# Kernel optimization log

Measured on AMD Instinct MI355X. Metric: run time of the kernel, lower is better.

The kernel has to match this reference:

```python
import jax, jax.numpy as jnp
import numpy as np
from jax import lax

B, S, E, SD = 8, 4096, 1024, 8


def setup_inputs() -> dict:
    key = jax.random.key(0)
    ks = jax.random.split(key, 4)
    x = jax.random.normal(ks[0], (B, S, E), dtype=jnp.float32)
    W_in = jax.random.normal(ks[1], (E, E + SD), dtype=jnp.float32) / np.sqrt(E)
    b_in = jnp.zeros((E + SD,), dtype=jnp.float32)
    W_g = jax.random.normal(ks[2], (E + SD, SD), dtype=jnp.float32) / np.sqrt(E + SD)
    b_g = jnp.zeros((SD,), dtype=jnp.float32)
    W_out = jax.random.normal(ks[3], (E + SD, E), dtype=jnp.float32) / np.sqrt(E + SD)
    b_out = jnp.zeros((E,), dtype=jnp.float32)
    return {"x": x, "W_in": W_in, "b_in": b_in, "W_g": W_g, "b_g": b_g,
            "W_out": W_out, "b_out": b_out}


def reference(x, W_in, b_in, W_g, b_g, W_out, b_out):
    embed_dim = W_in.shape[0]
    # State-independent projections batched over the whole sequence.
    combined = jnp.einsum('bse,ec->bsc', x, W_in) + b_in            # [B,S,E+SD]
    embed = combined[..., :embed_dim]                                # [B,S,E]
    state_in = combined[..., embed_dim:]                             # [B,S,SD]
    gate = jax.nn.sigmoid(jnp.einsum('bsc,cd->bsd', combined, W_g) + b_g)  # [B,S,SD]

    # Only the tiny gated state recurrence is sequential.
    def step(state, gs):
        g, si = gs
        new = g * state + (1.0 - g) * si
        return new, new

    state0 = jnp.zeros((x.shape[0], state_in.shape[-1]), dtype=x.dtype)
    g_t = jnp.moveaxis(gate, 1, 0)        # [S,B,SD]
    si_t = jnp.moveaxis(state_in, 1, 0)   # [S,B,SD]
    final_state, states = lax.scan(step, state0, (g_t, si_t))
    states = jnp.moveaxis(states, 0, 1)   # [B,S,SD]

    out = jnp.einsum('bsc,cd->bsd', jnp.concatenate([embed, states], axis=-1), W_out) + b_out
    return out, final_state
```

## Files before the change

kernel.cpp:

```cpp
#include <hip/hip_runtime.h>

typedef unsigned short ushort_t;
typedef __attribute__((ext_vector_type(8))) short short8;
typedef __attribute__((ext_vector_type(4))) float floatx4;

#define B_ 8
#define S_ 4096
#define E_ 1024
#define SD_ 8
#define M_TOTAL (B_ * S_)
#define NC 1032
#define NPAD 1152

__device__ __forceinline__ ushort_t f2bf(float f) {
    union { float f; unsigned u; } v; v.f = f;
    unsigned u = v.u;
    unsigned r = (u + 0x7fffu + ((u >> 16) & 1u)) >> 16;
    return (ushort_t)r;
}
__device__ __forceinline__ float bf2f(ushort_t h) {
    union { unsigned u; float f; } v; v.u = ((unsigned)h) << 16;
    return v.f;
}

__device__ __forceinline__ void stage16(ushort_t* lds_base_uniform, const ushort_t* g) {
#if __has_builtin(__builtin_amdgcn_global_load_lds)
    __builtin_amdgcn_global_load_lds(
        (const __attribute__((address_space(1))) void*)g,
        (__attribute__((address_space(3))) void*)lds_base_uniform, 16, 0, 0);
#else
    int lane = threadIdx.x & 63;
    *(short8*)((ushort_t*)lds_base_uniform + lane * 8) = *(const short8*)g;
#endif
}

__global__ void cvt_x4(const float* __restrict__ x, ushort_t* __restrict__ xb) {
    size_t i = ((size_t)blockIdx.x * 256 + threadIdx.x) * 4;
    float4 v = *(const float4*)(x + i);
    ushort4 o;
    o.x = f2bf(v.x); o.y = f2bf(v.y); o.z = f2bf(v.z); o.w = f2bf(v.w);
    *(ushort4*)(xb + i) = o;
}

__global__ void prep_win(const float* __restrict__ W, ushort_t* __restrict__ WT) {
    int idx = blockIdx.x * 256 + threadIdx.x;
    int n = idx >> 10, k = idx & 1023;
    WT[idx] = (n < NC) ? f2bf(W[(size_t)k * NC + n]) : (ushort_t)0;
}

__global__ void prep_wout(const float* __restrict__ W, ushort_t* __restrict__ WT) {
    int idx = blockIdx.x * 256 + threadIdx.x;
    int n = idx / NPAD, k = idx - n * NPAD;
    WT[idx] = (k < NC) ? f2bf(W[(size_t)k * E_ + n]) : (ushort_t)0;
}

template <bool OUT_BF16>
__global__ __launch_bounds__(256, 2) void gemm_bt(
    const ushort_t* __restrict__ A, const ushort_t* __restrict__ BT,
    void* __restrict__ Cout, const float* __restrict__ bias,
    int K, int lda, int ldb, int ldc, int nbias)
{
    __shared__ __align__(16) ushort_t sA[128 * 32];
    __shared__ __align__(16) ushort_t sB[128 * 32];
    const int tid = threadIdx.x;
    const int wave = tid >> 6;
    const int lane = tid & 63;
    const int m0 = blockIdx.y * 128;
    const int n0 = blockIdx.x * 128;
    const int wm = wave >> 1, wn = wave & 1;
    const int fr = lane & 15, fq = lane >> 4;
    const int sr = lane >> 2;
    const int sc = (lane & 3) * 8;

    floatx4 acc[4][4];
#pragma unroll
    for (int i = 0; i < 4; i++)
#pragma unroll
        for (int j = 0; j < 4; j++) acc[i][j] = (floatx4)0.f;

    const ushort_t* gA = A + (size_t)(m0 + wave * 32 + sr) * lda + sc;
    const ushort_t* gB = BT + (size_t)(n0 + wave * 32 + sr) * ldb + sc;

    for (int k0 = 0; k0 < K; k0 += 32) {
        __syncthreads();
        stage16(&sA[(wave * 32 + 0) * 32], gA + k0);
        stage16(&sA[(wave * 32 + 16) * 32], gA + (size_t)16 * lda + k0);
        stage16(&sB[(wave * 32 + 0) * 32], gB + k0);
        stage16(&sB[(wave * 32 + 16) * 32], gB + (size_t)16 * ldb + k0);
        __syncthreads();

        short8 a[4], b[4];
#pragma unroll
        for (int i = 0; i < 4; i++)
            a[i] = *(const short8*)&sA[(wm * 64 + i * 16 + fr) * 32 + fq * 8];
#pragma unroll
        for (int j = 0; j < 4; j++)
            b[j] = *(const short8*)&sB[(wn * 64 + j * 16 + fr) * 32 + fq * 8];
#pragma unroll
        for (int i = 0; i < 4; i++)
#pragma unroll
            for (int j = 0; j < 4; j++)
                acc[i][j] = __builtin_amdgcn_mfma_f32_16x16x32_bf16(a[i], b[j], acc[i][j], 0, 0, 0);
    }

#pragma unroll
    for (int i = 0; i < 4; i++) {
        int row = m0 + wm * 64 + i * 16 + fq * 4;
#pragma unroll
        for (int j = 0; j < 4; j++) {
            int col = n0 + wn * 64 + j * 16 + fr;
            float bv = (col < nbias) ? bias[col] : 0.f;
#pragma unroll
            for (int r = 0; r < 4; r++) {
                float v = acc[i][j][r] + bv;
                if (OUT_BF16)
                    ((ushort_t*)Cout)[(size_t)(row + r) * ldc + col] = f2bf(v);
                else
                    ((float*)Cout)[(size_t)(row + r) * ldc + col] = v;
            }
        }
    }
}

__global__ __launch_bounds__(256) void gate_kernel(
    const ushort_t* __restrict__ combined, const float* __restrict__ Wg,
    const float* __restrict__ bg, float* __restrict__ gate)
{
    __shared__ float WgT[8 * NPAD];
    const int tid = threadIdx.x;
    for (int idx = tid; idx < 8 * NPAD; idx += 256) {
        int d = idx / NPAD, c = idx - d * NPAD;
        WgT[idx] = (c < NC) ? Wg[(size_t)c * 8 + d] : 0.f;
    }
    __syncthreads();
    const int wave = tid >> 6, lane = tid & 63;
    for (int rr = 0; rr < 8; rr++) {
        int m = blockIdx.x * 32 + wave * 8 + rr;
        const ushort_t* crow = combined + (size_t)m * NPAD;
        float acc[8] = {0.f, 0.f, 0.f, 0.f, 0.f, 0.f, 0.f, 0.f};
        for (int i = 0; i < 18; i++) {
            float xv = bf2f(crow[i * 64 + lane]);
#pragma unroll
            for (int d = 0; d < 8; d++) acc[d] += xv * WgT[d * NPAD + i * 64 + lane];
        }
#pragma unroll
        for (int d = 0; d < 8; d++) {
#pragma unroll
            for (int off = 32; off >= 1; off >>= 1) acc[d] += __shfl_xor(acc[d], off);
        }
        if (lane == 0) {
#pragma unroll
            for (int d = 0; d < 8; d++) {
                float z = acc[d] + bg[d];
                gate[(size_t)m * 8 + d] = 1.f / (1.f + expf(-z));
            }
        }
    }
}

__global__ void scan_chunks(const float* __restrict__ gate, const ushort_t* __restrict__ combined,
                            float* __restrict__ chA, float* __restrict__ chB)
{
    const int c = blockIdx.x, lane = threadIdx.x;
    const int b = lane >> 3, d = lane & 7;
    float A = 1.f, Bv = 0.f;
    const int s0 = c * 64;
    for (int s = s0; s < s0 + 64; s++) {
        size_t m = (size_t)b * S_ + s;
        float g = gate[m * 8 + d];
        float si = bf2f(combined[m * NPAD + E_ + d]);
        Bv = g * Bv + (1.f - g) * si;
        A *= g;
    }
    chA[c * 64 + lane] = A;
    chB[c * 64 + lane] = Bv;
}

__global__ void scan_apply(const float* __restrict__ gate, ushort_t* __restrict__ combined,
                           const float* __restrict__ chA, const float* __restrict__ chB,
                           float* __restrict__ final_state)
{
    const int c = blockIdx.x, lane = threadIdx.x;
    const int b = lane >> 3, d = lane & 7;
    float state = 0.f;
    for (int j = 0; j < c; j++)
        state = chA[j * 64 + lane] * state + chB[j * 64 + lane];
    const int s0 = c * 64;
    for (int s = s0; s < s0 + 64; s++) {
        size_t m = (size_t)b * S_ + s;
        float g = gate[m * 8 + d];
        float si = bf2f(combined[m * NPAD + E_ + d]);
        state = g * state + (1.f - g) * si;
        combined[m * NPAD + E_ + d] = f2bf(state);
    }
    if (c == 63) final_state[lane] = state;
}

extern "C" void kernel_launch(void* const* d_in, const int* in_sizes, int n_in,
                              void* d_out, int out_size, void* d_ws, size_t ws_size,
                              hipStream_t stream)
{
    (void)in_sizes; (void)n_in; (void)out_size; (void)ws_size;
    const float* x     = (const float*)d_in[0];
    const float* W_in  = (const float*)d_in[1];
    const float* b_in  = (const float*)d_in[2];
    const float* W_g   = (const float*)d_in[3];
    const float* b_g   = (const float*)d_in[4];
    const float* W_out = (const float*)d_in[5];
    const float* b_out = (const float*)d_in[6];

    ushort_t* combined = (ushort_t*)d_ws;
    ushort_t* WinT  = combined + (size_t)M_TOTAL * NPAD;
    ushort_t* WoutT = WinT + (size_t)NPAD * E_;
    float* gate = (float*)(WoutT + (size_t)E_ * NPAD);
    float* chA  = gate + (size_t)M_TOTAL * SD_;
    float* chB  = chA + 64 * 64;

    ushort_t* xb = (ushort_t*)d_out;
    float* outp = (float*)d_out;
    float* fs = outp + (size_t)M_TOTAL * E_;

    cvt_x4<<<(M_TOTAL * E_) / 1024, 256, 0, stream>>>(x, xb);
    prep_win<<<(NPAD * E_) / 256, 256, 0, stream>>>(W_in, WinT);
    prep_wout<<<(E_ * NPAD) / 256, 256, 0, stream>>>(W_out, WoutT);

    gemm_bt<true><<<dim3(NPAD / 128, M_TOTAL / 128), 256, 0, stream>>>(
        xb, WinT, combined, b_in, E_, E_, E_, NPAD, NC);

    gate_kernel<<<M_TOTAL / 32, 256, 0, stream>>>(combined, W_g, b_g, gate);
    scan_chunks<<<64, 64, 0, stream>>>(gate, combined, chA, chB);
    scan_apply<<<64, 64, 0, stream>>>(gate, combined, chA, chB, fs);

    gemm_bt<false><<<dim3(E_ / 128, M_TOTAL / 128), 256, 0, stream>>>(
        combined, WoutT, outp, b_out, NPAD, NPAD, NPAD, E_, E_);
}
```

Baseline: 549.3 us.

## Fold gate projection into input GEMM via precomputed W_in·W_g columns

Precomputes W_in@W_g and the matching bias, then appends them as 8 extra output columns of the first GEMM, using spare padding columns. This removes the separate gate kernel, which re-read the whole combined matrix, and the float gate buffer. The scan kernels now apply the sigmoid themselves to the bf16 logits. The GEMM also remaps block indices into bands of 8 row tiles to improve L2 reuse. The risk is that the gate logits are now computed through a bf16-rounded fused weight, which changes numerics slightly.

```diff
diff --git a/kernel.cpp b/kernel.cpp
--- a/kernel.cpp
+++ b/kernel.cpp
@@ -10,6 +10,7 @@
 #define SD_ 8
 #define M_TOTAL (B_ * S_)
 #define NC 1032
+#define NG 1040
 #define NPAD 1152
 
 __device__ __forceinline__ ushort_t f2bf(float f) {
@@ -24,14 +25,9 @@
 }
 
 __device__ __forceinline__ void stage16(ushort_t* lds_base_uniform, const ushort_t* g) {
-#if __has_builtin(__builtin_amdgcn_global_load_lds)
     __builtin_amdgcn_global_load_lds(
         (const __attribute__((address_space(1))) void*)g,
         (__attribute__((address_space(3))) void*)lds_base_uniform, 16, 0, 0);
-#else
-    int lane = threadIdx.x & 63;
-    *(short8*)((ushort_t*)lds_base_uniform + lane * 8) = *(const short8*)g;
-#endif
 }
 
 __global__ void cvt_x4(const float* __restrict__ x, ushort_t* __restrict__ xb) {
@@ -42,10 +38,51 @@
     *(ushort4*)(xb + i) = o;
 }
 
-__global__ void prep_win(const float* __restrict__ W, ushort_t* __restrict__ WT) {
+__global__ void wcomb_kernel(const float* __restrict__ W_in, const float* __restrict__ Wg,
+                             float* __restrict__ Wc) {
+    const int k = blockIdx.x;
+    const int lane = threadIdx.x;
+    float acc[8] = {0.f,0.f,0.f,0.f,0.f,0.f,0.f,0.f};
+    for (int c = lane; c < NC; c += 64) {
+        float w = W_in[(size_t)k * NC + c];
+#pragma unroll
+        for (int d = 0; d < 8; d++) acc[d] += w * Wg[(size_t)c * 8 + d];
+    }
+#pragma unroll
+    for (int d = 0; d < 8; d++) {
+#pragma unroll
+        for (int off = 32; off >= 1; off >>= 1) acc[d] += __shfl_xor(acc[d], off);
+    }
+    if (lane == 0) {
+#pragma unroll
+        for (int d = 0; d < 8; d++) Wc[k * 8 + d] = acc[d];
+    }
+}
+
+__global__ void bias_ext_kernel(const float* __restrict__ b_in, const float* __restrict__ Wg,
+                                const float* __restrict__ bg, float* __restrict__ be) {
+    int c = blockIdx.x * 256 + threadIdx.x;
+    if (c >= NPAD) return;
+    if (c < NC) { be[c] = b_in[c]; return; }
+    if (c < NG) {
+        int d = c - NC;
+        float s = bg[d];
+        for (int j = 0; j < NC; j++) s += b_in[j] * Wg[(size_t)j * 8 + d];
+        be[c] = s;
+        return;
+    }
+    be[c] = 0.f;
+}
+
+__global__ void prep_win(const float* __restrict__ W, const float* __restrict__ Wc,
+                         ushort_t* __restrict__ WT) {
     int idx = blockIdx.x * 256 + threadIdx.x;
     int n = idx >> 10, k = idx & 1023;
-    WT[idx] = (n < NC) ? f2bf(W[(size_t)k * NC + n]) : (ushort_t)0;
+    float v;
+    if (n < NC)       v = W[(size_t)k * NC + n];
+    else if (n < NG)  v = Wc[k * 8 + (n - NC)];
+    else              v = 0.f;
+    WT[idx] = f2bf(v);
 }
 
 __global__ void prep_wout(const float* __restrict__ W, ushort_t* __restrict__ WT) {
@@ -58,15 +95,22 @@
 __global__ __launch_bounds__(256, 2) void gemm_bt(
     const ushort_t* __restrict__ A, const ushort_t* __restrict__ BT,
     void* __restrict__ Cout, const float* __restrict__ bias,
-    int K, int lda, int ldb, int ldc, int nbias)
+    int K, int lda, int ldb, int ldc)
 {
     __shared__ __align__(16) ushort_t sA[128 * 32];
     __shared__ __align__(16) ushort_t sB[128 * 32];
     const int tid = threadIdx.x;
     const int wave = tid >> 6;
     const int lane = tid & 63;
-    const int m0 = blockIdx.y * 128;
-    const int n0 = blockIdx.x * 128;
+
+    const int gx = gridDim.x;
+    int flat = blockIdx.y * gx + blockIdx.x;
+    const int band_size = 8 * gx;
+    int band = flat / band_size;
+    int r = flat - band * band_size;
+    const int m0 = (band * 8 + (r & 7)) * 128;
+    const int n0 = (r >> 3) * 128;
+
     const int wm = wave >> 1, wn = wave & 1;
     const int fr = lane & 15, fq = lane >> 4;
     const int sr = lane >> 2;
@@ -109,56 +153,20 @@
 #pragma unroll
         for (int j = 0; j < 4; j++) {
             int col = n0 + wn * 64 + j * 16 + fr;
-            float bv = (col < nbias) ? bias[col] : 0.f;
-#pragma unroll
-            for (int r = 0; r < 4; r++) {
-                float v = acc[i][j][r] + bv;
+            float bv = bias[col];
+#pragma unroll
+            for (int r2 = 0; r2 < 4; r2++) {
+                float v = acc[i][j][r2] + bv;
                 if (OUT_BF16)
-                    ((ushort_t*)Cout)[(size_t)(row + r) * ldc + col] = f2bf(v);
+                    ((ushort_t*)Cout)[(size_t)(row + r2) * ldc + col] = f2bf(v);
                 else
-                    ((float*)Cout)[(size_t)(row + r) * ldc + col] = v;
+                    ((float*)Cout)[(size_t)(row + r2) * ldc + col] = v;
             }
         }
     }
 }
 
-__global__ __launch_bounds__(256) void gate_kernel(
-    const ushort_t* __restrict__ combined, const float* __restrict__ Wg,
-    const float* __restrict__ bg, float* __restrict__ gate)
-{
-    __shared__ float WgT[8 * NPAD];
-    const int tid = threadIdx.x;
-    for (int idx = tid; idx < 8 * NPAD; idx += 256) {
-        int d = idx / NPAD, c = idx - d * NPAD;
-        WgT[idx] = (c < NC) ? Wg[(size_t)c * 8 + d] : 0.f;
-    }
-    __syncthreads();
-    const int wave = tid >> 6, lane = tid & 63;
-    for (int rr = 0; rr < 8; rr++) {
-        int m = blockIdx.x * 32 + wave * 8 + rr;
-        const ushort_t* crow = combined + (size_t)m * NPAD;
-        float acc[8] = {0.f, 0.f, 0.f, 0.f, 0.f, 0.f, 0.f, 0.f};
-        for (int i = 0; i < 18; i++) {
-            float xv = bf2f(crow[i * 64 + lane]);
-#pragma unroll
-            for (int d = 0; d < 8; d++) acc[d] += xv * WgT[d * NPAD + i * 64 + lane];
-        }
-#pragma unroll
-        for (int d = 0; d < 8; d++) {
-#pragma unroll
-            for (int off = 32; off >= 1; off >>= 1) acc[d] += __shfl_xor(acc[d], off);
-        }
-        if (lane == 0) {
-#pragma unroll
-            for (int d = 0; d < 8; d++) {
-                float z = acc[d] + bg[d];
-                gate[(size_t)m * 8 + d] = 1.f / (1.f + expf(-z));
-            }
-        }
-    }
-}
-
-__global__ void scan_chunks(const float* __restrict__ gate, const ushort_t* __restrict__ combined,
+__global__ void scan_chunks(const ushort_t* __restrict__ combined,
                             float* __restrict__ chA, float* __restrict__ chB)
 {
     const int c = blockIdx.x, lane = threadIdx.x;
@@ -167,7 +175,8 @@
     const int s0 = c * 64;
     for (int s = s0; s < s0 + 64; s++) {
         size_t m = (size_t)b * S_ + s;
-        float g = gate[m * 8 + d];
+        float z = bf2f(combined[m * NPAD + NC + d]);
+        float g = 1.f / (1.f + __expf(-z));
         float si = bf2f(combined[m * NPAD + E_ + d]);
         Bv = g * Bv + (1.f - g) * si;
         A *= g;
@@ -176,7 +185,7 @@
     chB[c * 64 + lane] = Bv;
 }
 
-__global__ void scan_apply(const float* __restrict__ gate, ushort_t* __restrict__ combined,
+__global__ void scan_apply(ushort_t* __restrict__ combined,
                            const float* __restrict__ chA, const float* __restrict__ chB,
                            float* __restrict__ final_state)
 {
@@ -188,7 +197,8 @@
     const int s0 = c * 64;
     for (int s = s0; s < s0 + 64; s++) {
         size_t m = (size_t)b * S_ + s;
-        float g = gate[m * 8 + d];
+        float z = bf2f(combined[m * NPAD + NC + d]);
+        float g = 1.f / (1.f + __expf(-z));
         float si = bf2f(combined[m * NPAD + E_ + d]);
         state = g * state + (1.f - g) * si;
         combined[m * NPAD + E_ + d] = f2bf(state);
@@ -212,8 +222,9 @@
     ushort_t* combined = (ushort_t*)d_ws;
     ushort_t* WinT  = combined + (size_t)M_TOTAL * NPAD;
     ushort_t* WoutT = WinT + (size_t)NPAD * E_;
-    float* gate = (float*)(WoutT + (size_t)E_ * NPAD);
-    float* chA  = gate + (size_t)M_TOTAL * SD_;
+    float* Wc   = (float*)(WoutT + (size_t)E_ * NPAD);
+    float* be   = Wc + 1024 * 8;
+    float* chA  = be + NPAD;
     float* chB  = chA + 64 * 64;
 
     ushort_t* xb = (ushort_t*)d_out;
@@ -221,16 +232,17 @@
     float* fs = outp + (size_t)M_TOTAL * E_;
 
     cvt_x4<<<(M_TOTAL * E_) / 1024, 256, 0, stream>>>(x, xb);
-    prep_win<<<(NPAD * E_) / 256, 256, 0, stream>>>(W_in, WinT);
+    wcomb_kernel<<<E_, 64, 0, stream>>>(W_in, W_g, Wc);
+    bias_ext_kernel<<<(NPAD + 255) / 256, 256, 0, stream>>>(b_in, W_g, b_g, be);
+    prep_win<<<(NPAD * E_) / 256, 256, 0, stream>>>(W_in, Wc, WinT);
     prep_wout<<<(E_ * NPAD) / 256, 256, 0, stream>>>(W_out, WoutT);
 
     gemm_bt<true><<<dim3(NPAD / 128, M_TOTAL / 128), 256, 0, stream>>>(
-        xb, WinT, combined, b_in, E_, E_, E_, NPAD, NC);
-
-    gate_kernel<<<M_TOTAL / 32, 256, 0, stream>>>(combined, W_g, b_g, gate);
-    scan_chunks<<<64, 64, 0, stream>>>(gate, combined, chA, chB);
-    scan_apply<<<64, 64, 0, stream>>>(gate, combined, chA, chB, fs);
+        xb, WinT, combined, be, E_, E_, E_, NPAD);
+
+    scan_chunks<<<64, 64, 0, stream>>>(combined, chA, chB);
+    scan_apply<<<64, 64, 0, stream>>>(combined, chA, chB, fs);
 
     gemm_bt<false><<<dim3(E_ / 128, M_TOTAL / 128), 256, 0, stream>>>(
-        combined, WoutT, outp, b_out, NPAD, NPAD, NPAD, E_, E_);
-}
+        combined, WoutT, outp, b_out, NPAD, NPAD, NPAD, E_);
+}
```

Measured after the change: 499.1 us. 9.1% less time.
